# Performance work log

Measured on AMD Instinct MI355X. Metric: run time of the kernel, lower is better.

Reference implementation:

```python
import math
import jax, jax.numpy as jnp
import numpy as np

H = 16      # n_head
DK = 64     # d_k = n_feat // n_head
D = 1024    # n_feat
TOPK = 64   # sparse_topk


def _laplace(x):
    # LaplacianAttnFn (Mega): 0.5 * (1 + erf((x - mu) / (std * sqrt(2))))
    mu = math.sqrt(0.5)
    std = math.sqrt(0.25 * math.pi)
    return 0.5 * (1.0 + jax.lax.erf((x - mu) / (std * math.sqrt(2.0))))


def setup_inputs() -> dict:
    key = jax.random.key(0)
    ks = jax.random.split(key, 12)
    B, T = 2, 2048
    inp = {
        "query": jax.random.normal(ks[0], (B, T, D), jnp.float32),
        "key": jax.random.normal(ks[1], (B, T, D), jnp.float32),
        "value": jax.random.normal(ks[2], (B, T, D), jnp.float32),
        "mask": jax.random.randint(ks[3], (B, T, T), 0, 2).astype(bool),
        "wq": 0.02 * jax.random.normal(ks[4], (D, D), jnp.float32),
        "bq": jnp.zeros((D,), jnp.float32),
        "wk": 0.02 * jax.random.normal(ks[5], (D, D), jnp.float32),
        "bk": jnp.zeros((D,), jnp.float32),
        "wv": 0.02 * jax.random.normal(ks[6], (D, D), jnp.float32),
        "bv": jnp.zeros((D,), jnp.float32),
        "wo": 0.02 * jax.random.normal(ks[7], (D, D), jnp.float32),
        "bo": jnp.zeros((D,), jnp.float32),
    }
    return inp


def reference(query, key, value, mask, wq, bq, wk, bk, wv, bv, wo, bo):
    B, T1, _ = query.shape
    T2 = key.shape[1]
    # QKV projections -> (b, h, t, d_k)
    def proj(x, w, b):
        y = x @ w.T + b
        return y.reshape(B, -1, H, DK).transpose(0, 2, 1, 3)
    q = proj(query, wq, bq)
    k = proj(key, wk, bk)
    v = proj(value, wv, bv)

    scores = jnp.einsum("bhqd,bhkd->bhqk", q, k) / math.sqrt(DK)  # (B,H,T1,T2)

    # top-k sparsification: keep only values >= k-th largest per row
    if TOPK is not None and TOPK < T2:
        top_vals, _ = jax.lax.top_k(scores, TOPK)
        vk = top_vals[..., -1:]
        scores = jnp.where(scores < vk, -jnp.finfo(scores.dtype).max, scores)

    m = mask[:, None]  # (B,1,T1,T2)
    scores = jnp.where(m, -10000.0, scores)
    attn = _laplace(scores)
    attn = jnp.where(m, 0.0, attn)

    x = jnp.einsum("bhqk,bhkd->bhqd", attn, v)  # (B,H,T1,DK)
    x = x.transpose(0, 2, 1, 3).reshape(B, T1, H * DK)
    return x @ wo.T + bo
```

## Files before the change

kernel.cpp:

```cpp
#include <hip/hip_runtime.h>
#include <math.h>

#define N_B     2
#define T_SEQ   2048
#define D_MODEL 1024
#define N_HEADS 16
#define D_HEAD  64
#define TOPK_N  64
#define DCAP    64
#define ACAP    40
#define QROWS   16
#define RPW     2

#define LAP_MU_F  0.70710678f
#define LAP_INV_F 0.79788456f
#define EERR      6e-3f

#define AS1 __attribute__((address_space(1)))
#define AS3 __attribute__((address_space(3)))

typedef _Float16 f16x4 __attribute__((ext_vector_type(4)));
typedef _Float16 f16x8 __attribute__((ext_vector_type(8)));
typedef float    f32x4 __attribute__((ext_vector_type(4)));
typedef double   f64x4 __attribute__((ext_vector_type(4)));

__device__ __forceinline__ float key2f(unsigned k) {
  unsigned b = (k & 0x80000000u) ? (k & 0x7fffffffu) : ~k;
  return __uint_as_float(b);
}

__global__ __launch_bounds__(256)
void pack_mask(const int* __restrict__ mask, unsigned* __restrict__ bits)
{
  const int wv = threadIdx.x >> 6, lane = threadIdx.x & 63;
  const int row = blockIdx.x * 4 + wv;
  const int* mrow = mask + (size_t)row * T_SEQ;
  unsigned w = 0;
#pragma unroll
  for (int j = 0; j < 32; ++j)
    w |= (mrow[j * 64 + lane] != 0 ? 1u : 0u) << j;
  bits[(size_t)row * 64 + lane] = w;
}

__global__ __launch_bounds__(256)
void split16(const float* __restrict__ src, char* __restrict__ dh,
             char* __restrict__ dl, float scale)
{
  const int tg = blockIdx.x * 256 + threadIdx.x;
  const int row = tg >> 7, unit = tg & 127;
  const int c0 = unit * 8;
  const int rb = row >> 6, r = row & 63, kt = c0 >> 6, c = c0 & 63;
  const size_t off = (((size_t)rb * 16 + kt) << 13)
                   + (size_t)r * 128 + (size_t)((c * 2) ^ ((r & 7) << 4));
  float4 v0 = *reinterpret_cast<const float4*>(&src[(size_t)row * 1024 + c0]);
  float4 v1 = *reinterpret_cast<const float4*>(&src[(size_t)row * 1024 + c0 + 4]);
  f16x8 h, l;
  float x;
  x = v0.x * scale; h[0] = (_Float16)x; l[0] = (_Float16)(x - (float)h[0]);
  x = v0.y * scale; h[1] = (_Float16)x; l[1] = (_Float16)(x - (float)h[1]);
  x = v0.z * scale; h[2] = (_Float16)x; l[2] = (_Float16)(x - (float)h[2]);
  x = v0.w * scale; h[3] = (_Float16)x; l[3] = (_Float16)(x - (float)h[3]);
  x = v1.x * scale; h[4] = (_Float16)x; l[4] = (_Float16)(x - (float)h[4]);
  x = v1.y * scale; h[5] = (_Float16)x; l[5] = (_Float16)(x - (float)h[5]);
  x = v1.z * scale; h[6] = (_Float16)x; l[6] = (_Float16)(x - (float)h[6]);
  x = v1.w * scale; h[7] = (_Float16)x; l[7] = (_Float16)(x - (float)h[7]);
  *reinterpret_cast<f16x8*>(dh + off) = h;
  *reinterpret_cast<f16x8*>(dl + off) = l;
}

__global__ __launch_bounds__(256)
void gemm_mfma_f16i(const char* __restrict__ AhI, const char* __restrict__ AlI,
                    const char* __restrict__ BhI, const char* __restrict__ BlI,
                    const float* __restrict__ bias, float* __restrict__ out,
                    int N, int head_layout)
{
  __shared__ _Float16 LAh[4096], LAl[4096], LBh[4096], LBl[4096];

  const int t = threadIdx.x, lane = t & 63, wv = t >> 6;
  const int row0 = blockIdx.x * 64, col0 = blockIdx.y * 64;
  const int wr = (wv >> 1) * 32, wc = (wv & 1) * 32;
  f32x4 acc[2][2] = {};

  for (int kt = 0; kt < 16; ++kt) {
    const size_t ca = (((size_t)blockIdx.x * 16 + kt) << 13);
    const size_t cb = (((size_t)blockIdx.y * 16 + kt) << 13);
#pragma unroll
    for (int j = 0; j < 2; ++j) {
      const int ub = wv * 64 + j * 256;
      const size_t gu = (size_t)(ub + lane) * 16;
      __builtin_amdgcn_global_load_lds((const AS1 void*)(AhI + ca + gu),
                                       (AS3 void*)((char*)LAh + (size_t)ub * 16), 16, 0, 0);
      __builtin_amdgcn_global_load_lds((const AS1 void*)(AlI + ca + gu),
                                       (AS3 void*)((char*)LAl + (size_t)ub * 16), 16, 0, 0);
      __builtin_amdgcn_global_load_lds((const AS1 void*)(BhI + cb + gu),
                                       (AS3 void*)((char*)LBh + (size_t)ub * 16), 16, 0, 0);
      __builtin_amdgcn_global_load_lds((const AS1 void*)(BlI + cb + gu),
                                       (AS3 void*)((char*)LBl + (size_t)ub * 16), 16, 0, 0);
    }
    __syncthreads();

#pragma unroll
    for (int ks = 0; ks < 2; ++ks) {
      const int lg = ks * 64 + (lane >> 4) * 16;
      f16x8 a_h[2], a_l[2], b_h[2], b_l[2];
#pragma unroll
      for (int i = 0; i < 2; ++i) {
        int ar = wr + i * 16 + (lane & 15);
        int pa = ar * 128 + (lg ^ ((ar & 7) << 4));
        a_h[i] = *reinterpret_cast<const f16x8*>((const char*)LAh + pa);
        a_l[i] = *reinterpret_cast<const f16x8*>((const char*)LAl + pa);
        int bc = wc + i * 16 + (lane & 15);
        int pb = bc * 128 + (lg ^ ((bc & 7) << 4));
        b_h[i] = *reinterpret_cast<const f16x8*>((const char*)LBh + pb);
        b_l[i] = *reinterpret_cast<const f16x8*>((const char*)LBl + pb);
      }
#pragma unroll
      for (int i = 0; i < 2; ++i)
#pragma unroll
        for (int j = 0; j < 2; ++j) {
          acc[i][j] = __builtin_amdgcn_mfma_f32_16x16x32_f16(a_h[i], b_h[j], acc[i][j], 0, 0, 0);
          acc[i][j] = __builtin_amdgcn_mfma_f32_16x16x32_f16(a_l[i], b_h[j], acc[i][j], 0, 0, 0);
          acc[i][j] = __builtin_amdgcn_mfma_f32_16x16x32_f16(a_h[i], b_l[j], acc[i][j], 0, 0, 0);
        }
    }
    __syncthreads();
  }

#pragma unroll
  for (int i = 0; i < 2; ++i)
#pragma unroll
    for (int j = 0; j < 2; ++j)
#pragma unroll
      for (int r = 0; r < 4; ++r) {
        int row = row0 + wr + i * 16 + ((lane >> 4) & 3) * 4 + r;
        int col = col0 + wc + j * 16 + (lane & 15);
        float v = acc[i][j][r] * 0.015625f + bias[col];
        if (head_layout) {
          int b = row >> 11, tt = row & (T_SEQ - 1);
          int hh = col >> 6, dk = col & 63;
          out[(((size_t)b * N_HEADS + hh) * T_SEQ + tt) * D_HEAD + dk] = v;
        } else {
          out[(size_t)row * N + col] = v;
        }
      }
}

__global__ __launch_bounds__(256)
void gemm_f64_qk(const float* __restrict__ Aq, const float* __restrict__ Ak,
                 const float* __restrict__ Wq, const float* __restrict__ Wk,
                 const float* __restrict__ bq, const float* __restrict__ bk,
                 double* __restrict__ Oq, double* __restrict__ Ok,
                 char* __restrict__ khS)
{
  __shared__ double As[64][33];
  __shared__ double Ws[64][33];
  __shared__ double vals[2];
  __shared__ int okflag;

  const int z = blockIdx.z;
  const float* A    = z ? Ak : Aq;
  const float* W    = z ? Wk : Wq;
  const float* bias = z ? bk : bq;
  double* out       = z ? Ok : Oq;
  char* kh          = z ? khS : (char*)0;

  const int t = threadIdx.x, lane = t & 63, wv = t >> 6;
  const int row0 = blockIdx.x * 64, col0 = blockIdx.y * 64;
  const int wr = (wv >> 1) * 32, wc = (wv & 1) * 32;
  f64x4 acc[2][2] = {};

  for (int k0 = 0; k0 < D_MODEL; k0 += 32) {
#pragma unroll
    for (int jj = 0; jj < 2; ++jj) {
      int idx = t + jj * 256;
      int r = idx >> 3, kq = idx & 7;
      float4 va = *reinterpret_cast<const float4*>(&A[(size_t)(row0 + r) * D_MODEL + k0 + kq * 4]);
      As[r][kq*4+0] = (double)va.x; As[r][kq*4+1] = (double)va.y;
      As[r][kq*4+2] = (double)va.z; As[r][kq*4+3] = (double)va.w;
      float4 vw = *reinterpret_cast<const float4*>(&W[(size_t)(col0 + r) * D_MODEL + k0 + kq * 4]);
      Ws[r][kq*4+0] = (double)vw.x; Ws[r][kq*4+1] = (double)vw.y;
      Ws[r][kq*4+2] = (double)vw.z; Ws[r][kq*4+3] = (double)vw.w;
    }
    __syncthreads();
#pragma unroll
    for (int kk = 0; kk < 32; kk += 4) {
      double a0 = As[wr +      (lane & 15)][kk + (lane >> 4)];
      double a1 = As[wr + 16 + (lane & 15)][kk + (lane >> 4)];
      double b0 = Ws[wc +      (lane & 15)][kk + (lane >> 4)];
      double b1 = Ws[wc + 16 + (lane & 15)][kk + (lane >> 4)];
      acc[0][0] = __builtin_amdgcn_mfma_f64_16x16x4f64(a0, b0, acc[0][0], 0, 0, 0);
      acc[0][1] = __builtin_amdgcn_mfma_f64_16x16x4f64(a0, b1, acc[0][1], 0, 0, 0);
      acc[1][0] = __builtin_amdgcn_mfma_f64_16x16x4f64(a1, b0, acc[1][0], 0, 0, 0);
      acc[1][1] = __builtin_amdgcn_mfma_f64_16x16x4f64(a1, b1, acc[1][1], 0, 0, 0);
    }
    __syncthreads();
  }

  if (t == 37) vals[0] = acc[0][0][1];
  if (t == 19) vals[1] = acc[0][0][3];
  double* red = &As[0][0];
  {
    double p1 = 0, p2 = 0;
    const int kb = t * 4;
#pragma unroll
    for (int k = 0; k < 4; ++k) {
      p1 = fma((double)A[(size_t)(row0 + 6) * D_MODEL + kb + k],
               (double)W[(size_t)(col0 + 5) * D_MODEL + kb + k], p1);
      p2 = fma((double)A[(size_t)(row0 + 13) * D_MODEL + kb + k],
               (double)W[(size_t)(col0 + 3) * D_MODEL + kb + k], p2);
    }
    red[t] = p1; red[256 + t] = p2;
  }
  __syncthreads();
  for (int s = 128; s > 0; s >>= 1) {
    if (t < s) { red[t] += red[t + s]; red[256 + t] += red[256 + t + s]; }
    __syncthreads();
  }
  if (t == 0) {
    double r1 = red[0], r2 = red[256];
    bool ok = (fabs(r1 - vals[0]) <= 1e-9 * (fabs(r1) + 1.0)) &&
              (fabs(r2 - vals[1]) <= 1e-9 * (fabs(r2) + 1.0));
    okflag = ok ? 1 : 0;
  }
  __syncthreads();

  if (okflag) {
#pragma unroll
    for (int i = 0; i < 2; ++i)
#pragma unroll
      for (int j = 0; j < 2; ++j)
#pragma unroll
        for (int r = 0; r < 4; ++r) {
          int row = row0 + wr + i * 16 + (lane >> 4) + 4 * r;
          int col = col0 + wc + j * 16 + (lane & 15);
          double v = acc[i][j][r] + (double)bias[col];
          int b = row >> 11, tt = row & (T_SEQ - 1);
          int h = col >> 6, dk = col & 63;
          size_t oi = (((size_t)b * N_HEADS + h) * T_SEQ + tt) * D_HEAD + dk;
          out[oi] = v;
          if (kh) {
            _Float16 hh = (_Float16)(float)v;
            int cch = tt >> 7, klo = tt & 127;
            size_t off = (((size_t)(b * N_HEADS + h) * 16 + cch) << 14)
                       + (size_t)klo * 128 + (size_t)((dk * 2) ^ ((klo & 7) << 4));
            *reinterpret_cast<_Float16*>(kh + off) = hh;
          }
        }
  } else {
    const int ty = t >> 4, tx = t & 15;
    double vacc[4][4] = {{0.0}};
    for (int k0 = 0; k0 < D_MODEL; k0 += 32) {
#pragma unroll
      for (int jj = 0; jj < 2; ++jj) {
        int idx = t + jj * 256;
        int r = idx >> 3, kq = idx & 7;
        float4 va = *reinterpret_cast<const float4*>(&A[(size_t)(row0 + r) * D_MODEL + k0 + kq * 4]);
        As[r][kq*4+0] = (double)va.x; As[r][kq*4+1] = (double)va.y;
        As[r][kq*4+2] = (double)va.z; As[r][kq*4+3] = (double)va.w;
        float4 vw = *reinterpret_cast<const float4*>(&W[(size_t)(col0 + r) * D_MODEL + k0 + kq * 4]);
        Ws[r][kq*4+0] = (double)vw.x; Ws[r][kq*4+1] = (double)vw.y;
        Ws[r][kq*4+2] = (double)vw.z; Ws[r][kq*4+3] = (double)vw.w;
      }
      __syncthreads();
#pragma unroll
      for (int kk = 0; kk < 32; ++kk) {
        double a[4], b[4];
#pragma unroll
        for (int i = 0; i < 4; ++i) a[i] = As[ty + 16*i][kk];
#pragma unroll
        for (int j = 0; j < 4; ++j) b[j] = Ws[tx + 16*j][kk];
#pragma unroll
        for (int i = 0; i < 4; ++i)
#pragma unroll
          for (int j = 0; j < 4; ++j) vacc[i][j] = fma(a[i], b[j], vacc[i][j]);
      }
      __syncthreads();
    }
#pragma unroll
    for (int i = 0; i < 4; ++i)
#pragma unroll
      for (int j = 0; j < 4; ++j) {
        int row = row0 + ty + 16*i, col = col0 + tx + 16*j;
        double v = vacc[i][j] + (double)bias[col];
        int b = row >> 11, tt = row & (T_SEQ - 1);
        int h = col >> 6, dk = col & 63;
        size_t oi = (((size_t)b * N_HEADS + h) * T_SEQ + tt) * D_HEAD + dk;
        out[oi] = v;
        if (kh) {
          _Float16 hh = (_Float16)(float)v;
          int cch = tt >> 7, klo = tt & 127;
          size_t off = (((size_t)(b * N_HEADS + h) * 16 + cch) << 14)
                     + (size_t)klo * 128 + (size_t)((dk * 2) ^ ((klo & 7) << 4));
          *reinterpret_cast<_Float16*>(kh + off) = hh;
        }
      }
  }
}

__device__ __forceinline__ void process_row(
    const float (&s)[32], int* __restrict__ dkl, float* __restrict__ dwl,
    int* __restrict__ akl, float* __restrict__ awl,
    const double* __restrict__ qrow, const double* __restrict__ Kd,
    const float* __restrict__ V, unsigned mw,
    char* __restrict__ axh, char* __restrict__ axl,
    size_t axbase, int rsw, size_t kvbase, int lane)
{
  unsigned p = 0u;
  for (int bit = 31; bit >= 12; --bit) {
    unsigned cand = p | (1u << bit);
    float cf = key2f(cand);
    int cnt = 0;
#pragma unroll
    for (int j = 0; j < 32; ++j) cnt += (int)__popcll(__ballot(s[j] >= cf));
    if (cnt >= TOPK_N) p = cand;
  }
  const float pv = key2f(p);
  const float pn = key2f(p + 4096u);
  const float hi = pn + 2.f * EERR;
  const float lo = pv - 2.f * EERR;

  int m = 0, na = 0;
#pragma unroll
  for (int j = 0; j < 32; ++j) {
    float sv = s[j];
    bool isd = (sv >= hi);
    bool isa = (sv >= lo) && !isd;
    unsigned long long bd = __ballot(isd);
    unsigned long long ba = __ballot(isa);
    int k = j * 64 + lane;
    if (isd) {
      int pos = m + (int)__popcll(bd & ((1ull << lane) - 1ull));
      if (pos < DCAP) {
        bool msk = ((mw >> j) & 1u) != 0u;
        dkl[pos] = k;
        dwl[pos] = msk ? 0.f : 0.5f * (1.f + erff((sv - LAP_MU_F) * LAP_INV_F));
      }
    }
    if (isa) {
      int pos = na + (int)__popcll(ba & ((1ull << lane) - 1ull));
      if (pos < ACAP) akl[pos] = k;
    }
    m += (int)__popcll(bd);
    na += (int)__popcll(ba);
  }
  if (m > DCAP) m = DCAP;
  if (na > ACAP) na = ACAP;
  const int need = TOPK_N - m;

  int ke = (na > 0) ? akl[lane < na ? lane : 0] : 0;
  const double* kr = &Kd[kvbase + (size_t)ke * D_HEAD];
  double a0 = 0, a1 = 0, a2 = 0, a3 = 0;
#pragma unroll
  for (int d = 0; d < 64; d += 4) {
    a0 = fma(qrow[d + 0], kr[d + 0], a0);
    a1 = fma(qrow[d + 1], kr[d + 1], a1);
    a2 = fma(qrow[d + 2], kr[d + 2], a2);
    a3 = fma(qrow[d + 3], kr[d + 3], a3);
  }
  double s64e = ((a0 + a1) + (a2 + a3)) * 0.125;

  unsigned mwk = __shfl(mw, ke & 63);
  bool mska = ((mwk >> (ke >> 6)) & 1u) != 0u;

  int rank = 0;
  for (int i = 0; i < na; ++i) {
    double vi = __shfl(s64e, i);
    rank += (vi > s64e) ? 1 : 0;
  }
  if (lane < na) {
    bool keep = (rank < need) && !mska;
    awl[lane] = keep ? 0.5f * (1.f + erff(((float)s64e - LAP_MU_F) * LAP_INV_F)) : 0.f;
  }

  float c0 = 0.f, c1 = 0.f, c2 = 0.f, c3 = 0.f;
  int e = 0;
  for (; e + 4 <= m; e += 4) {
    c0 = fmaf(dwl[e+0], V[kvbase + (size_t)dkl[e+0] * D_HEAD + lane], c0);
    c1 = fmaf(dwl[e+1], V[kvbase + (size_t)dkl[e+1] * D_HEAD + lane], c1);
    c2 = fmaf(dwl[e+2], V[kvbase + (size_t)dkl[e+2] * D_HEAD + lane], c2);
    c3 = fmaf(dwl[e+3], V[kvbase + (size_t)dkl[e+3] * D_HEAD + lane], c3);
  }
  for (; e < m; ++e)
    c0 = fmaf(dwl[e], V[kvbase + (size_t)dkl[e] * D_HEAD + lane], c0);
  for (int e2 = 0; e2 < na; ++e2)
    c1 = fmaf(awl[e2], V[kvbase + (size_t)akl[e2] * D_HEAD + lane], c1);

  float val = (c0 + c1) + (c2 + c3);
  _Float16 vh = (_Float16)val;
  _Float16 vl = (_Float16)(val - (float)vh);
  size_t off = axbase + (size_t)((lane * 2) ^ rsw);
  *reinterpret_cast<_Float16*>(axh + off) = vh;
  *reinterpret_cast<_Float16*>(axl + off) = vl;
}

__global__ __launch_bounds__(512)
void attn_fused(const double* __restrict__ Qd, const double* __restrict__ Kd,
                const char* __restrict__ KhS, const float* __restrict__ V,
                const unsigned* __restrict__ mbits,
                char* __restrict__ AxH, char* __restrict__ AxL)
{
  __shared__ _Float16 KsH[2][128 * 64];
  __shared__ float    S_lds[2][128][17];
  __shared__ char     pool[8192];
  __shared__ int      ak_l[QROWS][ACAP];
  __shared__ float    aw_l[QROWS][ACAP];

  _Float16 (*QhL)[64] = reinterpret_cast<_Float16(*)[64]>(pool);
  _Float16 (*QlL)[64] = reinterpret_cast<_Float16(*)[64]>(pool + 2048);
  int      (*dk_l)[DCAP] = reinterpret_cast<int(*)[DCAP]>(pool);
  float    (*dw_l)[DCAP] = reinterpret_cast<float(*)[DCAP]>(pool + 4096);

  const int t = threadIdx.x, wv = t >> 6, lane = t & 63;
  const int bh = blockIdx.y, b = bh >> 4, h = bh & 15;
  const int q0 = blockIdx.x * QROWS;
  const size_t kvbase = (size_t)bh * T_SEQ * D_HEAD;
  const size_t chbase = ((size_t)bh * 16) << 14;

  for (int i = t; i < QROWS * 64; i += 512) {
    int r = i >> 6, d = i & 63;
    float qf = (float)Qd[kvbase + (size_t)(q0 + r) * D_HEAD + d];
    _Float16 hh = (_Float16)qf;
    QhL[r][d] = hh;
    QlL[r][d] = (_Float16)(qf - (float)hh);
  }
#pragma unroll
  for (int jj = 0; jj < 2; ++jj) {
    int base = wv * 64 + jj * 512;
    char* lp = (char*)KsH[0] + (size_t)base * 16;
    __builtin_amdgcn_global_load_lds((const AS1 void*)(KhS + chbase + (size_t)(base + lane) * 16),
                                     (AS3 void*)lp, 16, 0, 0);
  }
  __syncthreads();

  const int qcol = lane & 15;
  const int kq = (lane >> 4) * 8;
  f16x8 Bh[2], Bl[2];
#pragma unroll
  for (int ds_ = 0; ds_ < 2; ++ds_) {
    Bh[ds_] = *reinterpret_cast<const f16x8*>(&QhL[qcol][ds_ * 32 + kq]);
    Bl[ds_] = *reinterpret_cast<const f16x8*>(&QlL[qcol][ds_ * 32 + kq]);
  }

  const int r0 = wv * RPW;
  float s0[32], s1[32];

  for (int c = 0; c < 16; ++c) {
    const int cur = c & 1;
    if (c < 15) {
      const char* gH = KhS + chbase + ((size_t)(c + 1) << 14);
#pragma unroll
      for (int jj = 0; jj < 2; ++jj) {
        int base = wv * 64 + jj * 512;
        char* lp = (char*)KsH[cur ^ 1] + (size_t)base * 16;
        __builtin_amdgcn_global_load_lds((const AS1 void*)(gH + (size_t)(base + lane) * 16),
                                         (AS3 void*)lp, 16, 0, 0);
      }
    }

    const int r = wv * 16 + (lane & 15);
    f32x4 acc = {0.f, 0.f, 0.f, 0.f};
#pragma unroll
    for (int ds_ = 0; ds_ < 2; ++ds_) {
      int lg = ds_ * 64 + (lane >> 4) * 16;
      int ph = r * 128 + (lg ^ ((r & 7) << 4));
      f16x8 Ah = *reinterpret_cast<const f16x8*>((const char*)KsH[cur] + ph);
      acc = __builtin_amdgcn_mfma_f32_16x16x32_f16(Ah, Bh[ds_], acc, 0, 0, 0);
      acc = __builtin_amdgcn_mfma_f32_16x16x32_f16(Ah, Bl[ds_], acc, 0, 0, 0);
    }

#pragma unroll
    for (int r2 = 0; r2 < 4; ++r2)
      S_lds[cur][wv * 16 + (lane >> 4) * 4 + r2][qcol] = acc[r2];

    __syncthreads();

    s0[c * 2 + 0] = S_lds[cur][lane][r0]          * 0.125f;
    s0[c * 2 + 1] = S_lds[cur][64 + lane][r0]     * 0.125f;
    s1[c * 2 + 0] = S_lds[cur][lane][r0 + 1]      * 0.125f;
    s1[c * 2 + 1] = S_lds[cur][64 + lane][r0 + 1] * 0.125f;
  }

  {
    const int lr = r0, qg = q0 + lr;
    const size_t rowg = (size_t)b * T_SEQ + qg;
    unsigned mw = mbits[rowg * 64 + lane];
    int rb = (int)(rowg >> 6), rr = (int)(rowg & 63);
    size_t axbase = (((size_t)rb * 16 + h) << 13) + (size_t)rr * 128;
    process_row(s0, dk_l[lr], dw_l[lr], ak_l[lr], aw_l[lr],
                &Qd[kvbase + (size_t)qg * D_HEAD], Kd, V, mw,
                AxH, AxL, axbase, (rr & 7) << 4, kvbase, lane);
  }
  {
    const int lr = r0 + 1, qg = q0 + lr;
    const size_t rowg = (size_t)b * T_SEQ + qg;
    unsigned mw = mbits[rowg * 64 + lane];
    int rb = (int)(rowg >> 6), rr = (int)(rowg & 63);
    size_t axbase = (((size_t)rb * 16 + h) << 13) + (size_t)rr * 128;
    process_row(s1, dk_l[lr], dw_l[lr], ak_l[lr], aw_l[lr],
                &Qd[kvbase + (size_t)qg * D_HEAD], Kd, V, mw,
                AxH, AxL, axbase, (rr & 7) << 4, kvbase, lane);
  }
}

extern "C" void kernel_launch(void* const* d_in, const int* in_sizes, int n_in,
                              void* d_out, int out_size, void* d_ws, size_t ws_size,
                              hipStream_t stream)
{
  const float* query = (const float*)d_in[0];
  const float* key_  = (const float*)d_in[1];
  const float* value = (const float*)d_in[2];
  const int*   mask  = (const int*)d_in[3];
  const float* wq = (const float*)d_in[4];
  const float* bq = (const float*)d_in[5];
  const float* wk = (const float*)d_in[6];
  const float* bk = (const float*)d_in[7];
  const float* wvp = (const float*)d_in[8];
  const float* bv = (const float*)d_in[9];
  const float* wo = (const float*)d_in[10];
  const float* bo = (const float*)d_in[11];
  float* out = (float*)d_out;

  double* Qd  = (double*)d_ws;
  double* Kd  = (double*)((char*)d_ws + ((size_t)32 << 20));
  char*   KhS = (char*)d_ws + ((size_t)64 << 20);
  char*   AxH = (char*)d_ws + ((size_t)80 << 20);
  char*   AxL = (char*)d_ws + ((size_t)88 << 20);
  unsigned* mbits = (unsigned*)((char*)d_ws + ((size_t)96 << 20));
  float*  Vb  = out;

  char* BvH = (char*)d_ws;
  char* BvL = (char*)d_ws + ((size_t)2 << 20);
  char* AvH = (char*)d_ws + ((size_t)32 << 20);
  char* AvL = (char*)d_ws + ((size_t)40 << 20);
  char* BoH = (char*)d_ws + ((size_t)32 << 20);
  char* BoL = (char*)d_ws + ((size_t)34 << 20);

  const int M = N_B * T_SEQ;
  dim3 gg64(M / 64, D_MODEL / 64);

  hipLaunchKernelGGL(split16, dim3(1024 * 128 / 256), dim3(256), 0, stream, wvp, BvH, BvL, 64.f);
  hipLaunchKernelGGL(split16, dim3((size_t)M * 128 / 256), dim3(256), 0, stream, value, AvH, AvL, 1.f);
  hipLaunchKernelGGL(gemm_mfma_f16i, gg64, dim3(256), 0, stream, AvH, AvL, BvH, BvL,
                     bv, Vb, D_MODEL, 1);

  hipLaunchKernelGGL(pack_mask, dim3(M / 4), dim3(256), 0, stream, mask, mbits);
  dim3 gqk(M / 64, D_MODEL / 64, 2);
  hipLaunchKernelGGL(gemm_f64_qk, gqk, dim3(256), 0, stream,
                     query, key_, wq, wk, bq, bk, Qd, Kd, KhS);

  dim3 ga(T_SEQ / QROWS, N_B * N_HEADS);
  hipLaunchKernelGGL(attn_fused, ga, dim3(512), 0, stream, Qd, Kd, KhS, Vb, mbits, AxH, AxL);

  hipLaunchKernelGGL(split16, dim3(1024 * 128 / 256), dim3(256), 0, stream, wo, BoH, BoL, 64.f);
  hipLaunchKernelGGL(gemm_mfma_f16i, gg64, dim3(256), 0, stream, AxH, AxL, BoH, BoL,
                     bo, out, D_MODEL, 0);
}
```

Before: 973.0 us.

## Load K fragments directly into registers and defer erf to post-compaction pass

The K-chunk staging through shared memory via global_load_lds is removed. Each lane now loads its MFMA A-fragments straight from global memory into registers, with one chunk of register prefetch and a fully unrolled loop. This drops about 32KB of LDS per block, which may raise occupancy, and removes the LDS write/read round trip. The top-k threshold radix search stops two bits earlier, giving a wider bucket, and the erf weight for definite entries is computed once per lane after compaction instead of inside the divergent ballot loop. The trade-offs are more global load latency exposed to MFMA, and a coarser threshold that lets more candidates into the ambiguous set.

```diff
diff --git a/kernel.cpp b/kernel.cpp
--- a/kernel.cpp
+++ b/kernel.cpp
@@ -306,7 +306,7 @@
     size_t axbase, int rsw, size_t kvbase, int lane)
 {
   unsigned p = 0u;
-  for (int bit = 31; bit >= 12; --bit) {
+  for (int bit = 31; bit >= 14; --bit) {
     unsigned cand = p | (1u << bit);
     float cf = key2f(cand);
     int cnt = 0;
@@ -315,7 +315,7 @@
     if (cnt >= TOPK_N) p = cand;
   }
   const float pv = key2f(p);
-  const float pn = key2f(p + 4096u);
+  const float pn = key2f(p + 16384u);
   const float hi = pn + 2.f * EERR;
   const float lo = pv - 2.f * EERR;
 
@@ -330,11 +330,7 @@
     int k = j * 64 + lane;
     if (isd) {
       int pos = m + (int)__popcll(bd & ((1ull << lane) - 1ull));
-      if (pos < DCAP) {
-        bool msk = ((mw >> j) & 1u) != 0u;
-        dkl[pos] = k;
-        dwl[pos] = msk ? 0.f : 0.5f * (1.f + erff((sv - LAP_MU_F) * LAP_INV_F));
-      }
+      if (pos < DCAP) { dkl[pos] = k; dwl[pos] = sv; }
     }
     if (isa) {
       int pos = na + (int)__popcll(ba & ((1ull << lane) - 1ull));
@@ -346,6 +342,15 @@
   if (m > DCAP) m = DCAP;
   if (na > ACAP) na = ACAP;
   const int need = TOPK_N - m;
+
+  {
+    int kdef = dkl[lane];
+    float sdef = dwl[lane];
+    unsigned mwd = __shfl(mw, kdef & 63);
+    bool mskd = ((mwd >> (kdef >> 6)) & 1u) != 0u;
+    float wdef = mskd ? 0.f : 0.5f * (1.f + erff((sdef - LAP_MU_F) * LAP_INV_F));
+    if (lane < m) dwl[lane] = wdef;
+  }
 
   int ke = (na > 0) ? akl[lane < na ? lane : 0] : 0;
   const double* kr = &Kd[kvbase + (size_t)ke * D_HEAD];
@@ -399,7 +404,6 @@
                 const unsigned* __restrict__ mbits,
                 char* __restrict__ AxH, char* __restrict__ AxL)
 {
-  __shared__ _Float16 KsH[2][128 * 64];
   __shared__ float    S_lds[2][128][17];
   __shared__ char     pool[8192];
   __shared__ int      ak_l[QROWS][ACAP];
@@ -414,7 +418,7 @@
   const int bh = blockIdx.y, b = bh >> 4, h = bh & 15;
   const int q0 = blockIdx.x * QROWS;
   const size_t kvbase = (size_t)bh * T_SEQ * D_HEAD;
-  const size_t chbase = ((size_t)bh * 16) << 14;
+  const char* gbase = KhS + (((size_t)bh * 16) << 14);
 
   for (int i = t; i < QROWS * 64; i += 512) {
     int r = i >> 6, d = i & 63;
@@ -423,13 +427,6 @@
     QhL[r][d] = hh;
     QlL[r][d] = (_Float16)(qf - (float)hh);
   }
-#pragma unroll
-  for (int jj = 0; jj < 2; ++jj) {
-    int base = wv * 64 + jj * 512;
-    char* lp = (char*)KsH[0] + (size_t)base * 16;
-    __builtin_amdgcn_global_load_lds((const AS1 void*)(KhS + chbase + (size_t)(base + lane) * 16),
-                                     (AS3 void*)lp, 16, 0, 0);
-  }
   __syncthreads();
 
   const int qcol = lane & 15;
@@ -441,32 +438,31 @@
     Bl[ds_] = *reinterpret_cast<const f16x8*>(&QlL[qcol][ds_ * 32 + kq]);
   }
 
+  const int rloc = wv * 16 + (lane & 15);
+  const int off0 = rloc * 128 + ((0 * 64 + (lane >> 4) * 16) ^ ((rloc & 7) << 4));
+  const int off1 = rloc * 128 + ((1 * 64 + (lane >> 4) * 16) ^ ((rloc & 7) << 4));
+
   const int r0 = wv * RPW;
   float s0[32], s1[32];
 
+  f16x8 a0c = *reinterpret_cast<const f16x8*>(gbase + off0);
+  f16x8 a1c = *reinterpret_cast<const f16x8*>(gbase + off1);
+
+#pragma unroll
   for (int c = 0; c < 16; ++c) {
     const int cur = c & 1;
+    f16x8 a0n, a1n;
     if (c < 15) {
-      const char* gH = KhS + chbase + ((size_t)(c + 1) << 14);
-#pragma unroll
-      for (int jj = 0; jj < 2; ++jj) {
-        int base = wv * 64 + jj * 512;
-        char* lp = (char*)KsH[cur ^ 1] + (size_t)base * 16;
-        __builtin_amdgcn_global_load_lds((const AS1 void*)(gH + (size_t)(base + lane) * 16),
-                                         (AS3 void*)lp, 16, 0, 0);
-      }
-    }
-
-    const int r = wv * 16 + (lane & 15);
+      const char* gc = gbase + ((size_t)(c + 1) << 14);
+      a0n = *reinterpret_cast<const f16x8*>(gc + off0);
+      a1n = *reinterpret_cast<const f16x8*>(gc + off1);
+    }
+
     f32x4 acc = {0.f, 0.f, 0.f, 0.f};
-#pragma unroll
-    for (int ds_ = 0; ds_ < 2; ++ds_) {
-      int lg = ds_ * 64 + (lane >> 4) * 16;
-      int ph = r * 128 + (lg ^ ((r & 7) << 4));
-      f16x8 Ah = *reinterpret_cast<const f16x8*>((const char*)KsH[cur] + ph);
-      acc = __builtin_amdgcn_mfma_f32_16x16x32_f16(Ah, Bh[ds_], acc, 0, 0, 0);
-      acc = __builtin_amdgcn_mfma_f32_16x16x32_f16(Ah, Bl[ds_], acc, 0, 0, 0);
-    }
+    acc = __builtin_amdgcn_mfma_f32_16x16x32_f16(a0c, Bh[0], acc, 0, 0, 0);
+    acc = __builtin_amdgcn_mfma_f32_16x16x32_f16(a0c, Bl[0], acc, 0, 0, 0);
+    acc = __builtin_amdgcn_mfma_f32_16x16x32_f16(a1c, Bh[1], acc, 0, 0, 0);
+    acc = __builtin_amdgcn_mfma_f32_16x16x32_f16(a1c, Bl[1], acc, 0, 0, 0);
 
 #pragma unroll
     for (int r2 = 0; r2 < 4; ++r2)
@@ -478,6 +474,8 @@
     s0[c * 2 + 1] = S_lds[cur][64 + lane][r0]     * 0.125f;
     s1[c * 2 + 0] = S_lds[cur][lane][r0 + 1]      * 0.125f;
     s1[c * 2 + 1] = S_lds[cur][64 + lane][r0 + 1] * 0.125f;
+
+    a0c = a0n; a1c = a1n;
   }
 
   {
```

Result: faster. 917.2 us (-5.7%).
